# Performance work log

Hardware: AMD Instinct MI355X
Metric: run time of the kernel (lower is better)

Reference implementation:

```python
import jax, jax.numpy as jnp
import numpy as np

# Model constants (from init_kwargs)
N_ATOMS = 30000
N_PAIRS = 300000
NF_IN = 64
NF_OUT = 64
N_DIST = 20
MIND_SOFT = 0.85
MAXD_SOFT = 5.0
HARD_CUTOFF = 6.5


def setup_inputs() -> dict:
    key = jax.random.key(0)
    k = jax.random.split(key, 8)
    in_features = jax.random.normal(k[0], (N_ATOMS, NF_IN), dtype=jnp.float32)
    pair_first = jax.random.randint(k[1], (N_PAIRS,), 0, N_ATOMS)
    pair_second = jax.random.randint(k[2], (N_PAIRS,), 0, N_ATOMS)
    dist_pairs = jax.random.uniform(k[3], (N_PAIRS,), dtype=jnp.float32,
                                    minval=MIND_SOFT, maxval=HARD_CUTOFF)
    # InverseSensitivityModule init: mu uniformly spaced in inverse-distance space
    mu = jnp.linspace(1.0 / MAXD_SOFT, 1.0 / MIND_SOFT, N_DIST, dtype=jnp.float32)
    sigma = jnp.full((N_DIST,), (1.0 / MIND_SOFT - 1.0 / MAXD_SOFT) / N_DIST,
                     dtype=jnp.float32)
    # xavier-normal-ish init scales
    int_weights = jax.random.normal(k[4], (N_DIST, NF_OUT, NF_IN), dtype=jnp.float32) \
        * np.sqrt(2.0 / (NF_IN + NF_OUT)).astype(np.float32)
    w_self = jax.random.normal(k[5], (NF_OUT, NF_IN), dtype=jnp.float32) \
        * np.sqrt(2.0 / (NF_IN + NF_OUT)).astype(np.float32)
    b_self = jax.random.normal(k[6], (NF_OUT,), dtype=jnp.float32) * 0.01
    return {"in_features": in_features, "pair_first": pair_first,
            "pair_second": pair_second, "dist_pairs": dist_pairs,
            "mu": mu, "sigma": sigma, "int_weights": int_weights,
            "w_self": w_self, "b_self": b_self}


def _sensitivity(dist, mu, sigma):
    # Inverse-distance Gaussian sensitivities with smooth cosine hard cutoff.
    inv_d = 1.0 / dist  # [P]
    gauss = jnp.exp(-0.5 * ((inv_d[:, None] - mu[None, :]) / sigma[None, :]) ** 2)  # [P, n_dist]
    cut = jnp.cos(0.5 * jnp.pi * dist / HARD_CUTOFF) ** 2
    cut = jnp.where(dist < HARD_CUTOFF, cut, 0.0)
    return gauss * cut[:, None]


def reference(in_features, pair_first, pair_second, dist_pairs,
              mu, sigma, int_weights, w_self, b_self):
    n_atoms = in_features.shape[0]
    sense = _sensitivity(dist_pairs, mu, sigma)              # [P, n_dist]
    # envsum: env[a, nu, f] = sum_{p: pair_first[p]==a} sense[p, nu] * in_features[pair_second[p], f]
    neigh = in_features[pair_second]                          # [P, nf_in] gather
    contrib = sense[:, :, None] * neigh[:, None, :]           # [P, n_dist, nf_in]
    env = jax.ops.segment_sum(
        contrib.reshape(contrib.shape[0], N_DIST * NF_IN),
        pair_first, num_segments=n_atoms)                     # [A, n_dist*nf_in]
    # interaction matmul: weights permuted (n_dist, nf_in, nf_out) then flattened
    weights_rs = jnp.transpose(int_weights, (0, 2, 1)).reshape(N_DIST * NF_IN, NF_OUT)
    features_out = env @ weights_rs                           # [A, nf_out]
    features_out += in_features @ w_self.T + b_self           # self interaction
    return features_out
```

## Files before the change

### kernel.cpp

```cpp
#include <hip/hip_runtime.h>
#include <math.h>

#define N_ATOMS    30000
#define N_PAIRS    300000
#define CAP        48
#define NF         64
#define ND         20
#define K_ENV      1280
#define K_TOT      1344
#define NKSTEP     42
#define HARD_CUT   6.5f
#define BA         16
#define ESTRIDE    1352
#define D_LO       0.85f
#define D_SCALE    (5.65f / 65535.0f)
#define D_SCALE_I  (65535.0f / 5.65f)
#define NM1        ((unsigned)(N_ATOMS - 1))

typedef short    s16x8  __attribute__((ext_vector_type(8)));
typedef __bf16   bf16x8 __attribute__((ext_vector_type(8)));
typedef unsigned u32x4  __attribute__((ext_vector_type(4)));
typedef float    f32x4  __attribute__((ext_vector_type(4)));
typedef float    f32x16 __attribute__((ext_vector_type(16)));

__device__ __forceinline__ unsigned short f2bf(float x) {
    union { float f; unsigned u; } v; v.f = x;
    unsigned r = v.u + 0x7fffu + ((v.u >> 16) & 1u);
    return (unsigned short)(r >> 16);
}
__device__ __forceinline__ unsigned pkbf(float a, float b) {
    return (unsigned)f2bf(a) | ((unsigned)f2bf(b) << 16);
}
__device__ __forceinline__ float senseval(unsigned pu, int kidx, int cnt,
                                          float isig, float musig, bool nuok) {
    float d  = D_LO + (float)(pu & 0xffffu) * D_SCALE;
    float z  = __builtin_amdgcn_rcpf(d) * isig - musig;
    float co = __cosf(0.2416609733530613f * d);
    float e  = __expf(-0.5f * z * z) * (co * co);
    return (nuok && kidx < cnt) ? e : 0.0f;
}

__global__ void k_prep(const float* __restrict__ iw, const float* __restrict__ wself,
                       const float* __restrict__ mu, const float* __restrict__ sigma,
                       const float* __restrict__ x,
                       unsigned short* __restrict__ WtB, int* __restrict__ cnts,
                       float2* __restrict__ msr, unsigned* __restrict__ xb16) {
    if (blockIdx.x < 42) {
        int idx = blockIdx.x * 256 + threadIdx.x;
        if (idx >= NKSTEP * 4 * 64) return;
        int l  = idx & 63;
        int q  = (idx >> 6) & 3;
        int ks = idx >> 8;
        int n  = q * 16 + (l & 15);
        int kb = ks * 32 + (l >> 4) * 8;
        u32x4 u;
        #pragma unroll
        for (int jj = 0; jj < 4; jj++) {
            unsigned short lo, hi;
            #pragma unroll
            for (int e = 0; e < 2; e++) {
                int k = kb + 2 * jj + e;
                float val;
                if (k < K_ENV) {
                    int t  = k / 640;
                    int rm = k - t * 640;
                    int g  = rm >> 7;
                    int c  = (rm & 127) >> 2;
                    int r  = k & 3;
                    int nu = 4 * g + r;
                    int f  = 2 * c + t;
                    val = iw[(nu * NF + n) * NF + f];
                } else {
                    val = wself[n * NF + (k - K_ENV)];
                }
                if (e == 0) lo = f2bf(val); else hi = f2bf(val);
            }
            u[jj] = (unsigned)lo | ((unsigned)hi << 16);
        }
        *(u32x4*)&WtB[idx * 8] = u;
    } else if (blockIdx.x < 160) {
        int i = (blockIdx.x - 42) * 256 + threadIdx.x;
        if (i < N_ATOMS) cnts[i] = 0;
    } else if (blockIdx.x == 160) {
        int i = threadIdx.x;
        if (i < ND) { float2 m; m.x = mu[i]; m.y = 1.0f / sigma[i]; msr[i] = m; }
    } else {
        int o = (blockIdx.x - 161) * 256 + threadIdx.x;
        if (o < N_ATOMS * 32 / 4) {
            int wbase = o * 4;
            const float* src = &x[(size_t)wbase * 2];
            float2 f0 = *(const float2*)(src);
            float2 f1 = *(const float2*)(src + 2);
            float2 f2 = *(const float2*)(src + 4);
            float2 f3 = *(const float2*)(src + 6);
            u32x4 u;
            u[0] = pkbf(f0.x, f0.y);
            u[1] = pkbf(f1.x, f1.y);
            u[2] = pkbf(f2.x, f2.y);
            u[3] = pkbf(f3.x, f3.y);
            *(u32x4*)&xb16[wbase] = u;
        }
    }
}

__global__ void k_scatter(const int* __restrict__ first, const int* __restrict__ second,
                          const float* __restrict__ dist, int* __restrict__ cnts,
                          unsigned* __restrict__ pk) {
    int p = (blockIdx.x * 256 + threadIdx.x) * 2;
    if (p >= N_PAIRS) return;
    int2   f2 = *(const int2*)&first[p];
    int2   s2 = *(const int2*)&second[p];
    float2 d2 = *(const float2*)&dist[p];
    {
        int pos = atomicAdd(&cnts[f2.x], 1);
        if (pos < CAP) {
            unsigned du = min((unsigned)((d2.x - D_LO) * D_SCALE_I + 0.5f), 65535u);
            pk[(size_t)f2.x * CAP + pos] = ((unsigned)s2.x << 16) | du;
        }
    }
    {
        int pos = atomicAdd(&cnts[f2.y], 1);
        if (pos < CAP) {
            unsigned du = min((unsigned)((d2.y - D_LO) * D_SCALE_I + 0.5f), 65535u);
            pk[(size_t)f2.y * CAP + pos] = ((unsigned)s2.y << 16) | du;
        }
    }
}

__global__ void __launch_bounds__(512, 6)
k_main(const unsigned* __restrict__ xb16, const int* __restrict__ cnts,
       const unsigned* __restrict__ pk, const float2* __restrict__ msr,
       const unsigned short* __restrict__ WtB, const float* __restrict__ bself,
       float* __restrict__ out) {
    __shared__ unsigned short env[BA * ESTRIDE];
    const int t  = threadIdx.x;
    const int w  = t >> 6;
    const int l  = t & 63;
    const int h  = l >> 5;
    const int cl = l & 31;
    const int a0 = blockIdx.x * BA;

    float2 ms   = msr[min(cl, ND - 1)];
    const float isig  = ms.y;
    const float musig = ms.x * ms.y;
    const bool  nuok  = (cl < ND);
    const unsigned* xw = xb16 + cl;

    #pragma unroll 1
    for (int ci = 0; ci < 2; ci++) {
        const int i = 2 * w + ci;
        const int a = a0 + i;
        const int cnt = min(cnts[a], CAP);
        const int nst = max((cnt + 15) >> 4, 1);
        const unsigned* gb = &pk[(size_t)a * CAP];
        f32x16 acc0 = {0.f}, acc1 = {0.f};
        #pragma unroll 1
        for (int ks = 0; ks < nst; ks++) {
            const int k0 = ks * 16 + h * 8;
            uint4 p0 = *(const uint4*)(gb + k0);
            uint4 p1 = *(const uint4*)(gb + k0 + 4);
            unsigned g0 = xw[min(p0.x >> 16, NM1) * 32];
            unsigned g1 = xw[min(p0.y >> 16, NM1) * 32];
            unsigned g2 = xw[min(p0.z >> 16, NM1) * 32];
            unsigned g3 = xw[min(p0.w >> 16, NM1) * 32];
            unsigned g4 = xw[min(p1.x >> 16, NM1) * 32];
            unsigned g5 = xw[min(p1.y >> 16, NM1) * 32];
            unsigned g6 = xw[min(p1.z >> 16, NM1) * 32];
            unsigned g7 = xw[min(p1.w >> 16, NM1) * 32];
            u32x4 A, B0, B1;
            A[0] = pkbf(senseval(p0.x, k0 + 0, cnt, isig, musig, nuok),
                        senseval(p0.y, k0 + 1, cnt, isig, musig, nuok));
            A[1] = pkbf(senseval(p0.z, k0 + 2, cnt, isig, musig, nuok),
                        senseval(p0.w, k0 + 3, cnt, isig, musig, nuok));
            A[2] = pkbf(senseval(p1.x, k0 + 4, cnt, isig, musig, nuok),
                        senseval(p1.y, k0 + 5, cnt, isig, musig, nuok));
            A[3] = pkbf(senseval(p1.z, k0 + 6, cnt, isig, musig, nuok),
                        senseval(p1.w, k0 + 7, cnt, isig, musig, nuok));
            B0[0] = __builtin_amdgcn_perm(g1, g0, 0x05040100u);
            B0[1] = __builtin_amdgcn_perm(g3, g2, 0x05040100u);
            B0[2] = __builtin_amdgcn_perm(g5, g4, 0x05040100u);
            B0[3] = __builtin_amdgcn_perm(g7, g6, 0x05040100u);
            B1[0] = __builtin_amdgcn_perm(g1, g0, 0x07060302u);
            B1[1] = __builtin_amdgcn_perm(g3, g2, 0x07060302u);
            B1[2] = __builtin_amdgcn_perm(g5, g4, 0x07060302u);
            B1[3] = __builtin_amdgcn_perm(g7, g6, 0x07060302u);
            acc0 = __builtin_amdgcn_mfma_f32_32x32x16_bf16(
                       __builtin_bit_cast(bf16x8, A),
                       __builtin_bit_cast(bf16x8, B0), acc0, 0, 0, 0);
            acc1 = __builtin_amdgcn_mfma_f32_32x32x16_bf16(
                       __builtin_bit_cast(bf16x8, A),
                       __builtin_bit_cast(bf16x8, B1), acc1, 0, 0, 0);
        }
        unsigned short* er = &env[i * ESTRIDE];
        #pragma unroll
        for (int q = 0; q < 3; q++) {
            int g = 2 * q + h;
            if (g < 5) {
                uint2 v0, v1;
                v0.x = pkbf(acc0[4 * q + 0], acc0[4 * q + 1]);
                v0.y = pkbf(acc0[4 * q + 2], acc0[4 * q + 3]);
                v1.x = pkbf(acc1[4 * q + 0], acc1[4 * q + 1]);
                v1.y = pkbf(acc1[4 * q + 2], acc1[4 * q + 3]);
                *(uint2*)&er[g * 128 + cl * 4]       = v0;
                *(uint2*)&er[640 + g * 128 + cl * 4] = v1;
            }
        }
        unsigned sw = xb16[(size_t)a * 32 + (l >> 1)];
        er[K_ENV + l] = (unsigned short)(sw >> ((l & 1) * 16));
    }
    __syncthreads();

    if (w < 4) {
        const int m16  = l & 15;
        const int quad = l >> 4;
        f32x4 acc = {0.f, 0.f, 0.f, 0.f};
        for (int ks = 0; ks < NKSTEP; ks++) {
            s16x8 afrag = *(const s16x8*)&env[m16 * ESTRIDE + ks * 32 + quad * 8];
            s16x8 bfrag = *(const s16x8*)&WtB[((ks * 4 + w) * 64 + l) * 8];
            acc = __builtin_amdgcn_mfma_f32_16x16x32_bf16(
                      __builtin_bit_cast(bf16x8, afrag),
                      __builtin_bit_cast(bf16x8, bfrag), acc, 0, 0, 0);
        }
        const float bs = bself[w * 16 + m16];
        #pragma unroll
        for (int r = 0; r < 4; r++) {
            int row = quad * 4 + r;
            out[(size_t)(a0 + row) * NF + w * 16 + m16] = acc[r] + bs;
        }
    }
}

extern "C" void kernel_launch(void* const* d_in, const int* in_sizes, int n_in,
                              void* d_out, int out_size, void* d_ws, size_t ws_size,
                              hipStream_t stream) {
    const float* x      = (const float*)d_in[0];
    const int*   first  = (const int*)d_in[1];
    const int*   second = (const int*)d_in[2];
    const float* dist   = (const float*)d_in[3];
    const float* mu     = (const float*)d_in[4];
    const float* sigma  = (const float*)d_in[5];
    const float* iw     = (const float*)d_in[6];
    const float* wself  = (const float*)d_in[7];
    const float* bself  = (const float*)d_in[8];
    float* out = (float*)d_out;

    char* ws = (char*)d_ws;
    unsigned short* WtB  = (unsigned short*)(ws);
    int*            cnts = (int*)(ws + 172032);
    float2*         msr  = (float2*)(ws + 292032);
    unsigned*       pk   = (unsigned*)(ws + 292192);
    unsigned*       xb16 = (unsigned*)(ws + 6052192);

    k_prep<<<dim3(161 + (N_ATOMS * 8 + 255) / 256), dim3(256), 0, stream>>>(
        iw, wself, mu, sigma, x, WtB, cnts, msr, xb16);
    k_scatter<<<dim3((N_PAIRS / 2 + 255) / 256), dim3(256), 0, stream>>>(
        first, second, dist, cnts, pk);
    k_main<<<dim3(N_ATOMS / BA), dim3(512), 0, stream>>>(
        xb16, cnts, pk, msr, WtB, bself, out);
}
```

Baseline: 125.0 us.

## One atom per wave, sentinel-padded neighbor lists, cheaper sensitivity math

Halves atoms per block to 8, so each wave builds a single atom's environment instead of looping over two, doubling the grid. Pre-fills the packed pair buffer with a sentinel word whose distance maps to the cutoff, giving near-zero sensitivity, so the per-element count and nu masks can be dropped. The sensitivity is rewritten with an exp2 whose scale is folded into mu/sigma, and a half-angle cosine in revolutions. bf16 packing uses a cheaper add-and-perm rounding. The cost is a large extra fill write in the prep kernel and half-empty 16-row MFMA tiles in the output stage.

```diff
diff --git a/kernel.cpp b/kernel.cpp
--- a/kernel.cpp
+++ b/kernel.cpp
@@ -9,13 +9,14 @@
 #define K_ENV      1280
 #define K_TOT      1344
 #define NKSTEP     42
-#define HARD_CUT   6.5f
-#define BA         16
+#define BA         8
 #define ESTRIDE    1352
 #define D_LO       0.85f
 #define D_SCALE    (5.65f / 65535.0f)
 #define D_SCALE_I  (65535.0f / 5.65f)
 #define NM1        ((unsigned)(N_ATOMS - 1))
+#define PAD_WORD   0x0000FFFFu
+#define GCONST     0.8493218f
 
 typedef short    s16x8  __attribute__((ext_vector_type(8)));
 typedef __bf16   bf16x8 __attribute__((ext_vector_type(8)));
@@ -31,20 +32,27 @@
 __device__ __forceinline__ unsigned pkbf(float a, float b) {
     return (unsigned)f2bf(a) | ((unsigned)f2bf(b) << 16);
 }
-__device__ __forceinline__ float senseval(unsigned pu, int kidx, int cnt,
-                                          float isig, float musig, bool nuok) {
-    float d  = D_LO + (float)(pu & 0xffffu) * D_SCALE;
-    float z  = __builtin_amdgcn_rcpf(d) * isig - musig;
-    float co = __cosf(0.2416609733530613f * d);
-    float e  = __expf(-0.5f * z * z) * (co * co);
-    return (nuok && kidx < cnt) ? e : 0.0f;
+__device__ __forceinline__ unsigned pkrh(float a, float b) {
+    unsigned ua = __builtin_bit_cast(unsigned, a) + 0x8000u;
+    unsigned ub = __builtin_bit_cast(unsigned, b) + 0x8000u;
+    return __builtin_amdgcn_perm(ub, ua, 0x07060302u);
+}
+__device__ __forceinline__ float senseq(unsigned pu, float slog, float nms) {
+    float uf  = (float)(pu & 0xffffu);
+    float d   = __builtin_fmaf(uf, D_SCALE, D_LO);
+    float inv = __builtin_amdgcn_rcpf(d);
+    float rev = __builtin_fmaf(uf, (float)(D_SCALE / 13.0f), D_LO / 13.0f);
+    float cut = __builtin_fmaf(__builtin_amdgcn_cosf(rev), 0.5f, 0.5f);
+    float zs  = __builtin_fmaf(inv, slog, nms);
+    return __builtin_amdgcn_exp2f(-(zs * zs)) * cut;
 }
 
 __global__ void k_prep(const float* __restrict__ iw, const float* __restrict__ wself,
                        const float* __restrict__ mu, const float* __restrict__ sigma,
                        const float* __restrict__ x,
                        unsigned short* __restrict__ WtB, int* __restrict__ cnts,
-                       float2* __restrict__ msr, unsigned* __restrict__ xb16) {
+                       float2* __restrict__ msr, unsigned* __restrict__ xb16,
+                       unsigned* __restrict__ pk) {
     if (blockIdx.x < 42) {
         int idx = blockIdx.x * 256 + threadIdx.x;
         if (idx >= NKSTEP * 4 * 64) return;
@@ -83,8 +91,14 @@
         if (i < N_ATOMS) cnts[i] = 0;
     } else if (blockIdx.x == 160) {
         int i = threadIdx.x;
-        if (i < ND) { float2 m; m.x = mu[i]; m.y = 1.0f / sigma[i]; msr[i] = m; }
-    } else {
+        if (i < ND) {
+            float isg = 1.0f / sigma[i];
+            float2 m;
+            m.y = isg * GCONST;
+            m.x = -mu[i] * isg * GCONST;
+            msr[i] = m;
+        }
+    } else if (blockIdx.x < 1099) {
         int o = (blockIdx.x - 161) * 256 + threadIdx.x;
         if (o < N_ATOMS * 32 / 4) {
             int wbase = o * 4;
@@ -100,6 +114,12 @@
             u[3] = pkbf(f3.x, f3.y);
             *(u32x4*)&xb16[wbase] = u;
         }
+    } else {
+        int o = (blockIdx.x - 1099) * 256 + threadIdx.x;
+        if (o < N_ATOMS * CAP / 4) {
+            u32x4 u = {PAD_WORD, PAD_WORD, PAD_WORD, PAD_WORD};
+            *(u32x4*)&pk[(size_t)o * 4] = u;
+        }
     }
 }
 
@@ -138,76 +158,66 @@
     const int l  = t & 63;
     const int h  = l >> 5;
     const int cl = l & 31;
-    const int a0 = blockIdx.x * BA;
-
-    float2 ms   = msr[min(cl, ND - 1)];
-    const float isig  = ms.y;
-    const float musig = ms.x * ms.y;
-    const bool  nuok  = (cl < ND);
+    const int a  = blockIdx.x * BA + w;
+
+    float2 ms = msr[min(cl, ND - 1)];
+    const float slog = ms.y;
+    const float nms  = ms.x;
     const unsigned* xw = xb16 + cl;
 
+    const int cnt = min(cnts[a], CAP);
+    const int nst = (cnt + 15) >> 4;
+    const unsigned* gb = &pk[(size_t)a * CAP];
+    f32x16 acc0 = {0.f}, acc1 = {0.f};
     #pragma unroll 1
-    for (int ci = 0; ci < 2; ci++) {
-        const int i = 2 * w + ci;
-        const int a = a0 + i;
-        const int cnt = min(cnts[a], CAP);
-        const int nst = max((cnt + 15) >> 4, 1);
-        const unsigned* gb = &pk[(size_t)a * CAP];
-        f32x16 acc0 = {0.f}, acc1 = {0.f};
-        #pragma unroll 1
-        for (int ks = 0; ks < nst; ks++) {
-            const int k0 = ks * 16 + h * 8;
-            uint4 p0 = *(const uint4*)(gb + k0);
-            uint4 p1 = *(const uint4*)(gb + k0 + 4);
-            unsigned g0 = xw[min(p0.x >> 16, NM1) * 32];
-            unsigned g1 = xw[min(p0.y >> 16, NM1) * 32];
-            unsigned g2 = xw[min(p0.z >> 16, NM1) * 32];
-            unsigned g3 = xw[min(p0.w >> 16, NM1) * 32];
-            unsigned g4 = xw[min(p1.x >> 16, NM1) * 32];
-            unsigned g5 = xw[min(p1.y >> 16, NM1) * 32];
-            unsigned g6 = xw[min(p1.z >> 16, NM1) * 32];
-            unsigned g7 = xw[min(p1.w >> 16, NM1) * 32];
-            u32x4 A, B0, B1;
-            A[0] = pkbf(senseval(p0.x, k0 + 0, cnt, isig, musig, nuok),
-                        senseval(p0.y, k0 + 1, cnt, isig, musig, nuok));
-            A[1] = pkbf(senseval(p0.z, k0 + 2, cnt, isig, musig, nuok),
-                        senseval(p0.w, k0 + 3, cnt, isig, musig, nuok));
-            A[2] = pkbf(senseval(p1.x, k0 + 4, cnt, isig, musig, nuok),
-                        senseval(p1.y, k0 + 5, cnt, isig, musig, nuok));
-            A[3] = pkbf(senseval(p1.z, k0 + 6, cnt, isig, musig, nuok),
-                        senseval(p1.w, k0 + 7, cnt, isig, musig, nuok));
-            B0[0] = __builtin_amdgcn_perm(g1, g0, 0x05040100u);
-            B0[1] = __builtin_amdgcn_perm(g3, g2, 0x05040100u);
-            B0[2] = __builtin_amdgcn_perm(g5, g4, 0x05040100u);
-            B0[3] = __builtin_amdgcn_perm(g7, g6, 0x05040100u);
-            B1[0] = __builtin_amdgcn_perm(g1, g0, 0x07060302u);
-            B1[1] = __builtin_amdgcn_perm(g3, g2, 0x07060302u);
-            B1[2] = __builtin_amdgcn_perm(g5, g4, 0x07060302u);
-            B1[3] = __builtin_amdgcn_perm(g7, g6, 0x07060302u);
-            acc0 = __builtin_amdgcn_mfma_f32_32x32x16_bf16(
-                       __builtin_bit_cast(bf16x8, A),
-                       __builtin_bit_cast(bf16x8, B0), acc0, 0, 0, 0);
-            acc1 = __builtin_amdgcn_mfma_f32_32x32x16_bf16(
-                       __builtin_bit_cast(bf16x8, A),
-                       __builtin_bit_cast(bf16x8, B1), acc1, 0, 0, 0);
-        }
-        unsigned short* er = &env[i * ESTRIDE];
-        #pragma unroll
-        for (int q = 0; q < 3; q++) {
-            int g = 2 * q + h;
-            if (g < 5) {
-                uint2 v0, v1;
-                v0.x = pkbf(acc0[4 * q + 0], acc0[4 * q + 1]);
-                v0.y = pkbf(acc0[4 * q + 2], acc0[4 * q + 3]);
-                v1.x = pkbf(acc1[4 * q + 0], acc1[4 * q + 1]);
-                v1.y = pkbf(acc1[4 * q + 2], acc1[4 * q + 3]);
-                *(uint2*)&er[g * 128 + cl * 4]       = v0;
-                *(uint2*)&er[640 + g * 128 + cl * 4] = v1;
-            }
-        }
-        unsigned sw = xb16[(size_t)a * 32 + (l >> 1)];
-        er[K_ENV + l] = (unsigned short)(sw >> ((l & 1) * 16));
-    }
+    for (int ks = 0; ks < nst; ks++) {
+        const int k0 = ks * 16 + h * 8;
+        uint4 p0 = *(const uint4*)(gb + k0);
+        uint4 p1 = *(const uint4*)(gb + k0 + 4);
+        unsigned g0 = xw[min(p0.x >> 16, NM1) * 32];
+        unsigned g1 = xw[min(p0.y >> 16, NM1) * 32];
+        unsigned g2 = xw[min(p0.z >> 16, NM1) * 32];
+        unsigned g3 = xw[min(p0.w >> 16, NM1) * 32];
+        unsigned g4 = xw[min(p1.x >> 16, NM1) * 32];
+        unsigned g5 = xw[min(p1.y >> 16, NM1) * 32];
+        unsigned g6 = xw[min(p1.z >> 16, NM1) * 32];
+        unsigned g7 = xw[min(p1.w >> 16, NM1) * 32];
+        u32x4 A, B0, B1;
+        A[0] = pkrh(senseq(p0.x, slog, nms), senseq(p0.y, slog, nms));
+        A[1] = pkrh(senseq(p0.z, slog, nms), senseq(p0.w, slog, nms));
+        A[2] = pkrh(senseq(p1.x, slog, nms), senseq(p1.y, slog, nms));
+        A[3] = pkrh(senseq(p1.z, slog, nms), senseq(p1.w, slog, nms));
+        B0[0] = __builtin_amdgcn_perm(g1, g0, 0x05040100u);
+        B0[1] = __builtin_amdgcn_perm(g3, g2, 0x05040100u);
+        B0[2] = __builtin_amdgcn_perm(g5, g4, 0x05040100u);
+        B0[3] = __builtin_amdgcn_perm(g7, g6, 0x05040100u);
+        B1[0] = __builtin_amdgcn_perm(g1, g0, 0x07060302u);
+        B1[1] = __builtin_amdgcn_perm(g3, g2, 0x07060302u);
+        B1[2] = __builtin_amdgcn_perm(g5, g4, 0x07060302u);
+        B1[3] = __builtin_amdgcn_perm(g7, g6, 0x07060302u);
+        acc0 = __builtin_amdgcn_mfma_f32_32x32x16_bf16(
+                   __builtin_bit_cast(bf16x8, A),
+                   __builtin_bit_cast(bf16x8, B0), acc0, 0, 0, 0);
+        acc1 = __builtin_amdgcn_mfma_f32_32x32x16_bf16(
+                   __builtin_bit_cast(bf16x8, A),
+                   __builtin_bit_cast(bf16x8, B1), acc1, 0, 0, 0);
+    }
+    unsigned short* er = &env[w * ESTRIDE];
+    #pragma unroll
+    for (int q = 0; q < 3; q++) {
+        int g = 2 * q + h;
+        if (g < 5) {
+            uint2 v0, v1;
+            v0.x = pkrh(acc0[4 * q + 0], acc0[4 * q + 1]);
+            v0.y = pkrh(acc0[4 * q + 2], acc0[4 * q + 3]);
+            v1.x = pkrh(acc1[4 * q + 0], acc1[4 * q + 1]);
+            v1.y = pkrh(acc1[4 * q + 2], acc1[4 * q + 3]);
+            *(uint2*)&er[g * 128 + cl * 4]       = v0;
+            *(uint2*)&er[640 + g * 128 + cl * 4] = v1;
+        }
+    }
+    unsigned sw = xb16[(size_t)a * 32 + (l >> 1)];
+    er[K_ENV + l] = (unsigned short)(sw >> ((l & 1) * 16));
     __syncthreads();
 
     if (w < 4) {
@@ -215,17 +225,19 @@
         const int quad = l >> 4;
         f32x4 acc = {0.f, 0.f, 0.f, 0.f};
         for (int ks = 0; ks < NKSTEP; ks++) {
-            s16x8 afrag = *(const s16x8*)&env[m16 * ESTRIDE + ks * 32 + quad * 8];
+            s16x8 afrag = *(const s16x8*)&env[(m16 & 7) * ESTRIDE + ks * 32 + quad * 8];
             s16x8 bfrag = *(const s16x8*)&WtB[((ks * 4 + w) * 64 + l) * 8];
             acc = __builtin_amdgcn_mfma_f32_16x16x32_bf16(
                       __builtin_bit_cast(bf16x8, afrag),
                       __builtin_bit_cast(bf16x8, bfrag), acc, 0, 0, 0);
         }
         const float bs = bself[w * 16 + m16];
+        const int a0 = blockIdx.x * BA;
         #pragma unroll
         for (int r = 0; r < 4; r++) {
             int row = quad * 4 + r;
-            out[(size_t)(a0 + row) * NF + w * 16 + m16] = acc[r] + bs;
+            if (row < BA)
+                out[(size_t)(a0 + row) * NF + w * 16 + m16] = acc[r] + bs;
         }
     }
 }
@@ -251,8 +263,8 @@
     unsigned*       pk   = (unsigned*)(ws + 292192);
     unsigned*       xb16 = (unsigned*)(ws + 6052192);
 
-    k_prep<<<dim3(161 + (N_ATOMS * 8 + 255) / 256), dim3(256), 0, stream>>>(
-        iw, wself, mu, sigma, x, WtB, cnts, msr, xb16);
+    k_prep<<<dim3(1099 + (N_ATOMS * CAP / 4 + 255) / 256), dim3(256), 0, stream>>>(
+        iw, wself, mu, sigma, x, WtB, cnts, msr, xb16, pk);
     k_scatter<<<dim3((N_PAIRS / 2 + 255) / 256), dim3(256), 0, stream>>>(
         first, second, dist, cnts, pk);
     k_main<<<dim3(N_ATOMS / BA), dim3(512), 0, stream>>>(
```

After: 130.9 us. 1.05x slower.
